# Kernel optimization log

Hardware: AMD Instinct MI355X
Metric: run time of the kernel (lower is better)

Reference implementation:

```python
import jax, jax.numpy as jnp
import numpy as np
import math

D_MODEL = 2048
NUM_HEADS = 32
NUM_KV_HEADS = 8
D_K = D_MODEL // NUM_HEADS  # 64
GROUPS = NUM_HEADS // NUM_KV_HEADS  # 4
WINDOW = 512
ROPE_BASE = 10000.0


def setup_inputs() -> dict:
    key = jax.random.key(0)
    ks = jax.random.split(key, 5)
    B, T = 2, 2048
    x = jax.random.normal(ks[0], (B, T, D_MODEL), dtype=jnp.float32)
    s = 0.02  # typical init scale to keep logits sane
    Wq = jax.random.normal(ks[1], (D_MODEL, D_MODEL), dtype=jnp.float32) * s
    Wk = jax.random.normal(ks[2], (NUM_KV_HEADS * D_K, D_MODEL), dtype=jnp.float32) * s
    Wv = jax.random.normal(ks[3], (NUM_KV_HEADS * D_K, D_MODEL), dtype=jnp.float32) * s
    Wo = jax.random.normal(ks[4], (D_MODEL, D_MODEL), dtype=jnp.float32) * s
    return {"x": x, "Wq": Wq, "Wk": Wk, "Wv": Wv, "Wo": Wo}


def _rotate_half(t):
    half = t.shape[-1] // 2
    return jnp.concatenate([-t[..., half:], t[..., :half]], axis=-1)


def _rope_cos_sin(T, dtype):
    inv_freq = 1.0 / (ROPE_BASE ** (jnp.arange(0, D_K, 2, dtype=jnp.float32) / D_K))
    pos = jnp.arange(T, dtype=jnp.float32)
    freqs = pos[:, None] * inv_freq[None, :]            # [T, D_K/2]
    emb = jnp.concatenate([freqs, freqs], axis=-1)       # [T, D_K]
    return jnp.cos(emb).astype(dtype)[None, None], jnp.sin(emb).astype(dtype)[None, None]


def reference(x, Wq, Wk, Wv, Wo):
    B, T, D = x.shape
    # Projections (nn.Linear: x @ W.T)
    Q = (x @ Wq.T).reshape(B, T, NUM_HEADS, D_K).transpose(0, 2, 1, 3)     # [B,H,T,dk]
    K = (x @ Wk.T).reshape(B, T, NUM_KV_HEADS, D_K).transpose(0, 2, 1, 3)  # [B,KV,T,dk]
    V = (x @ Wv.T).reshape(B, T, NUM_KV_HEADS, D_K).transpose(0, 2, 1, 3)
    # RoPE
    cos, sin = _rope_cos_sin(T, x.dtype)
    Q = Q * cos + _rotate_half(Q) * sin
    K = K * cos + _rotate_half(K) * sin
    # GQA: fold group dim into Q instead of repeat_interleave on K/V (same math)
    Qg = Q.reshape(B, NUM_KV_HEADS, GROUPS, T, D_K)
    scale = math.sqrt(D_K)
    scores = jnp.einsum('bhgqd,bhkd->bhgqk', Qg, K) / scale  # [B,KV,G,T,T]
    # sliding-window causal mask: valid iff 0 <= q_pos - k_pos < WINDOW
    pos = jnp.arange(T)
    dist = pos[:, None] - pos[None, :]
    win_mask = (dist < 0) | (dist >= WINDOW)
    scores = jnp.where(win_mask[None, None, None], -jnp.inf, scores)
    attn = jax.nn.softmax(scores, axis=-1)
    out = jnp.einsum('bhgqk,bhkd->bhgqd', attn, V)
    out = out.reshape(B, NUM_HEADS, T, D_K).transpose(0, 2, 1, 3).reshape(B, T, D)
    return out @ Wo.T
```

## Files before the change

kernel.cpp:

```cpp
#include <hip/hip_runtime.h>
#include <hip/hip_bf16.h>
#include <cstdint>
#include <cstddef>

typedef __attribute__((ext_vector_type(4))) float f32x4;
typedef __attribute__((ext_vector_type(8))) short bf16x8;
typedef __attribute__((ext_vector_type(4))) int i32x4;
typedef void __attribute__((address_space(1)))* as1_void_p;
typedef void __attribute__((address_space(3)))* as3_void_p;

#define T_SEQ 2048
#define D_MODEL 2048
#define NUM_HEADS 32
#define NUM_KV 8
#define GROUPS 4
#define DK 64
#define WINDOW 512
#define BATCH 2

#define NEG_BIG (-30000.0f)

__device__ __forceinline__ unsigned short f2b(float f) {
    unsigned int u = __builtin_bit_cast(unsigned int, f);
    u = (u + 0x7FFFu + ((u >> 16) & 1u)) >> 16;
    return (unsigned short)u;
}

__device__ __forceinline__ unsigned int cvtpk_bf16(float lo, float hi) {
    unsigned int r;
    asm("v_cvt_pk_bf16_f32 %0, %1, %2" : "=v"(r) : "v"(lo), "v"(hi));
    return r;
}

__device__ __forceinline__ void load_lds16(const void* g, void* l) {
    __builtin_amdgcn_global_load_lds((as1_void_p)(uintptr_t)g,
                                     (as3_void_p)(unsigned int)(uintptr_t)l,
                                     16, 0, 0);
}

#define CAST_N0 8388608
#define CAST_N1 12582912
#define CAST_N2 13631488
#define CAST_N3 14680064
#define CAST_N4 18874368
__global__ void cast_all_kernel(const float* __restrict__ x, const float* __restrict__ wq,
                                const float* __restrict__ wk, const float* __restrict__ wv,
                                const float* __restrict__ wo, unsigned short* __restrict__ dst) {
    int i = (blockIdx.x * blockDim.x + threadIdx.x) * 4;
    const int stride = gridDim.x * blockDim.x * 4;
    for (; i < CAST_N4; i += stride) {
        const float* src;
        int off;
        if (i < CAST_N0)      { src = x;  off = i; }
        else if (i < CAST_N1) { src = wq; off = i - CAST_N0; }
        else if (i < CAST_N2) { src = wk; off = i - CAST_N1; }
        else if (i < CAST_N3) { src = wv; off = i - CAST_N2; }
        else                  { src = wo; off = i - CAST_N3; }
        const float4 v = *(const float4*)(src + off);
        ushort4 o;
        o.x = f2b(v.x); o.y = f2b(v.y); o.z = f2b(v.z); o.w = f2b(v.w);
        *(ushort4*)(dst + i) = o;
    }
}

__global__ void rope_table_kernel(float* __restrict__ ct, float* __restrict__ st) {
    int i = blockIdx.x * blockDim.x + threadIdx.x;
    int t = i >> 5, j = i & 31;
    const float kln = 0.28782313662425556f;
    float inv = __expf(-(float)j * kln);
    if (j == 0) inv = 1.0f;
    float ang = (float)t * inv;
    float s, c;
    sincosf(ang, &s, &c);
    ct[i] = c; st[i] = s;
}


#define STAGE32(LDSOFF, SRC, ROWBASE, KCOL)                                    \
    { _Pragma("unroll") for (int u = 0; u < 2; ++u) {                          \
        const int gi = u * 512 + tid;                                          \
        const int row_ = gi >> 2, slot_ = gi & 3;                              \
        const int scol = (slot_ ^ ((row_ >> 1) & 3)) << 3;                     \
        load_lds16(SRC + (size_t)((ROWBASE) + row_) * 2048 + (KCOL) + scol,    \
                   (char*)&lds[LDSOFF] + gi * 16); } }

#define GEMM8_CORE(APTR, BPTR, TM, TN, AROWS, BROWS)                           \
    const int tid = threadIdx.x;                                               \
    const int lane = tid & 63;                                                 \
    const int wid = tid >> 6;                                                  \
    const int wr = wid >> 1, wc = wid & 1;                        \
    const int lrow = lane & 15;                                                \
    const int g = lane >> 4;                                                   \
    const int tile_m = (TM), tile_n = (TN);                                    \
    const int arow = tile_m * (AROWS), brow = tile_n * (BROWS);                \
    (void)brow;

__global__ __launch_bounds__(512, 2) void gemm_qkv_rope(
    const unsigned short* __restrict__ A, const unsigned short* __restrict__ Bw,
    const float* __restrict__ ct, const float* __restrict__ st,
    unsigned short* __restrict__ Qb, unsigned short* __restrict__ Kb,
    unsigned short* __restrict__ Vt) {
    __shared__ __align__(16) unsigned short lds[32768];
    const int bid = blockIdx.x;
    const int xcd = bid & 7;
    const int l = bid >> 3;
    const int stl = l >> 4;
    const int w = l & 15;
    const int tmD = xcd * 4 + (w >> 2);
    const int tnD = stl * 4 + (w & 3);

    GEMM8_CORE(A, Bw, tmD, tnD, 128, 128)

    const int srow = tid >> 2, sslot = tid & 3;
    const int scol0 = (sslot ^ ((srow >> 1) & 3)) << 3;

    f32x4 acc[2][4] = {};

#define QSTAGE(BUF, KCOL)                                                      \
    {                                                                          \
        load_lds16(A + (size_t)(arow + srow) * 2048 + (KCOL) + scol0,          \
                   (char*)&lds[(BUF) * 8192] + tid * 16);                      \
        load_lds16(Bw + (size_t)(tnD * 128 + srow) * 2048 + (KCOL) + scol0,    \
                   (char*)&lds[(BUF) * 8192 + 4096] + tid * 16);               \
    }

    QSTAGE(0, 0) QSTAGE(1, 32) QSTAGE(2, 64)
    asm volatile("s_waitcnt vmcnt(4)" ::: "memory");
    __builtin_amdgcn_sched_barrier(0);
    __builtin_amdgcn_s_barrier();

    for (int t = 0; t < 64; ++t) {
        const int cb = (t & 3) * 8192;
        const int sb = (t + 3) & 3;
        bf16x8 af[2], bfr[4];
#pragma unroll
        for (int m = 0; m < 2; ++m) {
            const int R = wr * 32 + m * 16 + lrow;
            af[m] = *(const bf16x8*)&lds[cb + R * 32 + ((g ^ ((R >> 1) & 3)) << 3)];
        }
#pragma unroll
        for (int n = 0; n < 4; ++n) {
            const int R = wc * 64 + n * 16 + lrow;
            bfr[n] = *(const bf16x8*)&lds[cb + 4096 + R * 32 + ((g ^ ((R >> 1) & 3)) << 3)];
        }
        if (t + 3 < 64) QSTAGE(sb, (t + 3) * 32)
        __builtin_amdgcn_s_barrier();
        asm volatile("s_waitcnt lgkmcnt(0)" ::: "memory");
        __builtin_amdgcn_sched_barrier(0);
        __builtin_amdgcn_s_setprio(1);
#pragma unroll
        for (int m = 0; m < 2; ++m)
#pragma unroll
            for (int n = 0; n < 4; ++n)
                acc[m][n] = __builtin_amdgcn_mfma_f32_16x16x32_bf16(af[m], bfr[n], acc[m][n], 0, 0, 0);
        __builtin_amdgcn_s_setprio(0);
        if (t < 63) { asm volatile("s_waitcnt vmcnt(4)" ::: "memory"); }
        else        { asm volatile("s_waitcnt vmcnt(0)" ::: "memory"); }
        __builtin_amdgcn_sched_barrier(0);
        __builtin_amdgcn_s_barrier();
    }
#undef QSTAGE

    const int hcol = tile_n * 2 + wc;
#pragma unroll
    for (int m = 0; m < 2; ++m) {
        const int row0 = tile_m * 128 + wr * 32 + m * 16 + g * 4;
        const int bb = row0 >> 11;
        const int t0 = row0 & 2047;
        if (hcol < 40) {
            const bool isQ = (hcol < 32);
            const float sc = isQ ? 0.125f : 1.0f;
            unsigned short* base = isQ
                ? (Qb + ((size_t)(bb * NUM_HEADS + hcol) * T_SEQ) * 64)
                : (Kb + ((size_t)(bb * NUM_KV + (hcol - 32)) * T_SEQ) * 64);
#pragma unroll
            for (int r = 0; r < 4; ++r) {
                const int t = t0 + r;
                unsigned short* dst = base + (size_t)t * 64;
#pragma unroll
                for (int n = 0; n < 2; ++n) {
                    const int j = n * 16 + lrow;
                    const float c = ct[t * 32 + j], s = st[t * 32 + j];
                    const float v0 = acc[m][n][r], v1 = acc[m][n + 2][r];
                    dst[j]      = f2b((v0 * c - v1 * s) * sc);
                    dst[j + 32] = f2b((v1 * c + v0 * s) * sc);
                }
            }
        } else {
            const int vh = hcol - 40;
            const int chunk = t0 >> 5, tk = t0 & 31;
            unsigned short* cbase = Vt + ((size_t)(bb * NUM_KV + vh) * 64 + chunk) * 2048 + tk;
#pragma unroll
            for (int n = 0; n < 4; ++n) {
                const int d = n * 16 + lrow;
                unsigned int u0 = cvtpk_bf16(acc[m][n][0], acc[m][n][1]);
                unsigned int u1 = cvtpk_bf16(acc[m][n][2], acc[m][n][3]);
                uint2 val; val.x = u0; val.y = u1;
                *(uint2*)(cbase + d * 32) = val;
            }
        }
    }
}

__global__ __launch_bounds__(512, 2) void gemm_bf16_nt(
    const unsigned short* __restrict__ A, const unsigned short* __restrict__ B,
    float* __restrict__ C) {
    __shared__ __align__(16) unsigned short lds[49152];
    const int bid = blockIdx.x;
    const int xcd = bid & 7;
    const int l = bid >> 3;
    const int stl = l >> 4;
    const int w = l & 15;
    const int tmD = xcd * 4 + (w >> 2);
    const int tnD = stl * 4 + (w & 3);

    const int tid = threadIdx.x;
    const int lane = tid & 63;
    const int wid = tid >> 6;
    const int wr = wid >> 2, wc = wid & 3;
    const int lrow = lane & 15;
    const int g = lane >> 4;
    const int tile_m = tmD, tile_n = tnD;
    const int arow = tile_m * 128, brow = tile_n * 256;

    const int srow = tid >> 2, sslot = tid & 3;
    const int scol = (sslot ^ ((srow >> 1) & 3)) << 3;

    f32x4 acc[4][4] = {};

#define OSTAGE(BUF, KCOL)                                                      \
    {                                                                          \
        load_lds16(A + (size_t)(arow + srow) * 2048 + (KCOL) + scol,           \
                   (char*)&lds[(BUF) * 12288] + tid * 16);                     \
        _Pragma("unroll") for (int u = 0; u < 2; ++u) {                        \
            const int gi = u * 512 + tid;                                      \
            const int br_ = gi >> 2, bs_ = gi & 3;                             \
            const int bc_ = (bs_ ^ ((br_ >> 1) & 3)) << 3;                     \
            load_lds16(B + (size_t)(brow + br_) * 2048 + (KCOL) + bc_,         \
                       (char*)&lds[(BUF) * 12288 + 4096] + gi * 16);           \
        }                                                                      \
    }

    OSTAGE(0, 0) OSTAGE(1, 32) OSTAGE(2, 64)
    asm volatile("s_waitcnt vmcnt(6)" ::: "memory");
    __builtin_amdgcn_sched_barrier(0);
    __builtin_amdgcn_s_barrier();

    for (int t = 0; t < 64; ++t) {
        const int cb = (t & 3) * 12288;
        const int sb = (t + 3) & 3;
        bf16x8 af[4], bfr[4];
#pragma unroll
        for (int m = 0; m < 4; ++m) {
            const int R = wr * 64 + m * 16 + lrow;
            af[m] = *(const bf16x8*)&lds[cb + R * 32 + ((g ^ ((R >> 1) & 3)) << 3)];
        }
#pragma unroll
        for (int n = 0; n < 4; ++n) {
            const int R = wc * 64 + n * 16 + lrow;
            bfr[n] = *(const bf16x8*)&lds[cb + 4096 + R * 32 + ((g ^ ((R >> 1) & 3)) << 3)];
        }
        if (t + 3 < 64) OSTAGE(sb, (t + 3) * 32)
        __builtin_amdgcn_s_barrier();
        asm volatile("s_waitcnt lgkmcnt(0)" ::: "memory");
        __builtin_amdgcn_sched_barrier(0);
        __builtin_amdgcn_s_setprio(1);
#pragma unroll
        for (int m = 0; m < 4; ++m)
#pragma unroll
            for (int n = 0; n < 4; ++n)
                acc[m][n] = __builtin_amdgcn_mfma_f32_16x16x32_bf16(af[m], bfr[n], acc[m][n], 0, 0, 0);
        __builtin_amdgcn_s_setprio(0);
        if (t < 63) { asm volatile("s_waitcnt vmcnt(6)" ::: "memory"); }
        else        { asm volatile("s_waitcnt vmcnt(0)" ::: "memory"); }
        __builtin_amdgcn_sched_barrier(0);
        __builtin_amdgcn_s_barrier();
    }
#undef OSTAGE

#pragma unroll
    for (int m = 0; m < 4; ++m)
#pragma unroll
        for (int n = 0; n < 4; ++n) {
            const int col = tile_n * 256 + wc * 64 + n * 16 + lrow;
#pragma unroll
            for (int r = 0; r < 4; ++r) {
                const int row = tile_m * 128 + wr * 64 + m * 16 + g * 4 + r;
                C[(size_t)row * 2048 + col] = acc[m][n][r];
            }
        }
}

__global__ __launch_bounds__(512, 2) void attn_kernel(
    const unsigned short* __restrict__ Qb, const unsigned short* __restrict__ Kb,
    const unsigned short* __restrict__ Vt, unsigned short* __restrict__ Oout) {
    __shared__ __align__(16) unsigned short lds[12288];
    const int tid = threadIdx.x;
    const int lane = tid & 63;
    const int wv = tid >> 6;
    const int g4 = wv & 3;
    const int tile = wv >> 2;
    const int bid = blockIdx.x;
    const int kvh = bid & 7;
    const int b = (bid >> 3) & 1;
    const int band = 63 - (bid >> 4);
    const int q0A = band * 32;
    const int q0w = q0A + tile * 16;
    const int h = kvh * 4 + g4;

    const int lq = lane & 15;
    const int g = lane >> 4;
    const int kq8 = g * 8;
    const int q = q0w + lq;

    const unsigned short* Qrow = Qb + ((size_t)((b * NUM_HEADS + h) * T_SEQ) + q) * 64;
    const bf16x8 qf0 = *(const bf16x8*)(Qrow + kq8);
    const bf16x8 qf1 = *(const bf16x8*)(Qrow + 32 + kq8);

    f32x4 acc[4] = {};
    float lrun = 0.0f;

    int kc_lo = q0A - (WINDOW - 1);
    if (kc_lo < 0) kc_lo = 0;
    kc_lo &= ~31;
    const int N = ((q0A - kc_lo) >> 5) + 1;

    const unsigned short* Kg = Kb + (size_t)(b * NUM_KV + kvh) * T_SEQ * 64
                                  + (size_t)kc_lo * 64;
    const unsigned short* Vg = Vt + (size_t)(b * NUM_KV + kvh) * 64 * T_SEQ
                                  + (size_t)(kc_lo >> 5) * 2048;

    const int perm = (lq >> 2) * 8 + (lq & 3);
#define SWZK(r) (((r & 3) | ((r >> 3) << 2)) & 7)
    const int koff0 = perm * 64 + ((g ^ SWZK(perm)) << 3);
    const int koff1 = perm * 64 + (((4 + g) ^ SWZK(perm)) << 3);
    const int perm4 = perm + 4;
    const int koff2 = perm4 * 64 + ((g ^ SWZK(perm4)) << 3);
    const int koff3 = perm4 * 64 + (((4 + g) ^ SWZK(perm4)) << 3);
    int voff[4];
#pragma unroll
    for (int nd = 0; nd < 4; ++nd)
        voff[nd] = 2048 + (nd * 16 + lq) * 32 + ((g ^ ((lq >> 1) & 3)) << 3);

#define STAGE(T, BUF)                                                          \
    {                                                                          \
        if (tid < 256) {                                                       \
            const int row_ = tid >> 3, ps = tid & 7;                           \
            const int ls = ps ^ SWZK(row_);                                    \
            load_lds16(Kg + (size_t)(T) * 2048 + row_ * 64 + ls * 8,           \
                       (char*)lds + (BUF) * 8192 + tid * 16);                  \
        } else {                                                               \
            const int gi = tid - 256;                                          \
            const int row_ = gi >> 2, ps = gi & 3;                             \
            const int ls = ps ^ ((row_ >> 1) & 3);                             \
            load_lds16(Vg + (size_t)(T) * 2048 + row_ * 32 + ls * 8,           \
                       (char*)lds + (BUF) * 8192 + 4096 + gi * 16);            \
        }                                                                      \
    }

    STAGE(0, 0)
    if (N > 1) {
        STAGE(1, 1)
        asm volatile("s_waitcnt vmcnt(1)" ::: "memory");
    } else {
        asm volatile("s_waitcnt vmcnt(0)" ::: "memory");
    }
    __builtin_amdgcn_sched_barrier(0);
    __builtin_amdgcn_s_barrier();

    int kb = 0;
    int sbuf = 2;
    for (int t = 0; t < N; ++t) {
        bf16x8 kf[4], vf[4];
        kf[0] = *(const bf16x8*)&lds[kb + koff0];
        kf[1] = *(const bf16x8*)&lds[kb + koff1];
        kf[2] = *(const bf16x8*)&lds[kb + koff2];
        kf[3] = *(const bf16x8*)&lds[kb + koff3];
#pragma unroll
        for (int nd = 0; nd < 4; ++nd) vf[nd] = *(const bf16x8*)&lds[kb + voff[nd]];
        if (t + 2 < N) STAGE(t + 2, sbuf)
        asm volatile("s_waitcnt lgkmcnt(0)" ::: "memory");
        __builtin_amdgcn_sched_barrier(0);

        const int kc = kc_lo + t * 32;
        f32x4 st2[2] = {};
        st2[0] = __builtin_amdgcn_mfma_f32_16x16x32_bf16(kf[0], qf0, st2[0], 0, 0, 0);
        st2[0] = __builtin_amdgcn_mfma_f32_16x16x32_bf16(kf[1], qf1, st2[0], 0, 0, 0);
        st2[1] = __builtin_amdgcn_mfma_f32_16x16x32_bf16(kf[2], qf0, st2[1], 0, 0, 0);
        st2[1] = __builtin_amdgcn_mfma_f32_16x16x32_bf16(kf[3], qf1, st2[1], 0, 0, 0);

        float s8[8];
#pragma unroll
        for (int tt = 0; tt < 2; ++tt)
#pragma unroll
            for (int r = 0; r < 4; ++r) s8[tt * 4 + r] = st2[tt][r];

        if (kc < q0w - 496 || kc > q0w - 31) {
#pragma unroll
            for (int i = 0; i < 8; ++i) {
                const int key = kc + g * 8 + ((i >> 2) << 2) + (i & 3);
                const int dist = q - key;
                if (dist < 0 || dist >= WINDOW) s8[i] = NEG_BIG;
            }
        }

        float p8[8];
        float ps = 0.0f;
#pragma unroll
        for (int i = 0; i < 8; ++i) {
            p8[i] = __expf(s8[i]);
            ps += p8[i];
        }
        lrun += ps;

        i32x4 pwi;
        pwi[0] = (int)cvtpk_bf16(p8[0], p8[1]);
        pwi[1] = (int)cvtpk_bf16(p8[2], p8[3]);
        pwi[2] = (int)cvtpk_bf16(p8[4], p8[5]);
        pwi[3] = (int)cvtpk_bf16(p8[6], p8[7]);
        const bf16x8 pw = __builtin_bit_cast(bf16x8, pwi);

#pragma unroll
        for (int nd = 0; nd < 4; ++nd)
            acc[nd] = __builtin_amdgcn_mfma_f32_16x16x32_bf16(vf[nd], pw, acc[nd], 0, 0, 0);

        if (t + 1 < N) {
            if (t + 2 < N) { asm volatile("s_waitcnt vmcnt(1)" ::: "memory"); }
            else           { asm volatile("s_waitcnt vmcnt(0)" ::: "memory"); }
            __builtin_amdgcn_sched_barrier(0);
            __builtin_amdgcn_s_barrier();
        }
        kb += 4096; if (kb == 12288) kb = 0;
        sbuf += 1;  if (sbuf == 3) sbuf = 0;
    }
#undef STAGE
#undef SWZK

    lrun += __shfl_xor(lrun, 16);
    lrun += __shfl_xor(lrun, 32);

    const float inv = 1.0f / lrun;
#pragma unroll
    for (int nd = 0; nd < 4; ++nd) {
        unsigned int u0 = cvtpk_bf16(acc[nd][0] * inv, acc[nd][1] * inv);
        unsigned int u1 = cvtpk_bf16(acc[nd][2] * inv, acc[nd][3] * inv);
        unsigned short* dst = Oout + ((size_t)(b * T_SEQ + q)) * D_MODEL + h * 64 + nd * 16 + g * 4;
        uint2 val; val.x = u0; val.y = u1;
        *(uint2*)dst = val;
    }
}

extern "C" void kernel_launch(void* const* d_in, const int* in_sizes, int n_in,
                              void* d_out, int out_size, void* d_ws, size_t ws_size,
                              hipStream_t stream) {
    const float* x = (const float*)d_in[0];
    const float* Wq = (const float*)d_in[1];
    const float* Wk = (const float*)d_in[2];
    const float* Wv = (const float*)d_in[3];
    const float* Wo = (const float*)d_in[4];
    float* out = (float*)d_out;

    char* ws = (char*)d_ws;
    size_t off = 0;
    auto alloc = [&](size_t bytes) -> char* {
        char* p = ws + off;
        off += (bytes + 255) & ~(size_t)255;
        return p;
    };
    unsigned short* xb   = (unsigned short*)alloc(8388608ull * 2);
    unsigned short* wcat = (unsigned short*)alloc(6291456ull * 2);
    unsigned short* wob  = (unsigned short*)alloc(4194304ull * 2);
    unsigned short* qb   = (unsigned short*)alloc(8388608ull * 2);
    unsigned short* kb   = (unsigned short*)alloc(2097152ull * 2);
    unsigned short* vt   = (unsigned short*)alloc(2097152ull * 2);
    unsigned short* attn = (unsigned short*)alloc(8388608ull * 2);
    float* ct            = (float*)alloc(65536ull * 4);
    float* st            = (float*)alloc(65536ull * 4);

    cast_all_kernel<<<2048, 256, 0, stream>>>(x, Wq, Wk, Wv, Wo, xb);
    rope_table_kernel<<<256, 256, 0, stream>>>(ct, st);

    gemm_qkv_rope<<<768, 512, 0, stream>>>(xb, wcat, ct, st, qb, kb, vt);

    attn_kernel<<<1024, 512, 0, stream>>>(qb, kb, vt, attn);

    gemm_bf16_nt<<<256, 512, 0, stream>>>(attn, wob, out);
}
```

Measured before the change: 153.6 us.

## Deepen attention K/V prefetch to four LDS buffers and raise occupancy bounds

The attention kernel's K/V staging ring grows from three to four LDS buffers, with tiles prefetched three steps ahead and the vmcnt waits adjusted to match. This is meant to hide more global load latency behind the MFMA and softmax work. Launch bounds for both the QKV GEMM and attention kernels are raised from 2 to 4 blocks per CU, which pushes the compiler to use fewer registers and may cause spills. The GEMM helper macros are also inlined, which does not change behaviour.

```diff
diff --git a/kernel.cpp b/kernel.cpp
--- a/kernel.cpp
+++ b/kernel.cpp
@@ -76,26 +76,7 @@
 }
 
 
-#define STAGE32(LDSOFF, SRC, ROWBASE, KCOL)                                    \
-    { _Pragma("unroll") for (int u = 0; u < 2; ++u) {                          \
-        const int gi = u * 512 + tid;                                          \
-        const int row_ = gi >> 2, slot_ = gi & 3;                              \
-        const int scol = (slot_ ^ ((row_ >> 1) & 3)) << 3;                     \
-        load_lds16(SRC + (size_t)((ROWBASE) + row_) * 2048 + (KCOL) + scol,    \
-                   (char*)&lds[LDSOFF] + gi * 16); } }
-
-#define GEMM8_CORE(APTR, BPTR, TM, TN, AROWS, BROWS)                           \
-    const int tid = threadIdx.x;                                               \
-    const int lane = tid & 63;                                                 \
-    const int wid = tid >> 6;                                                  \
-    const int wr = wid >> 1, wc = wid & 1;                        \
-    const int lrow = lane & 15;                                                \
-    const int g = lane >> 4;                                                   \
-    const int tile_m = (TM), tile_n = (TN);                                    \
-    const int arow = tile_m * (AROWS), brow = tile_n * (BROWS);                \
-    (void)brow;
-
-__global__ __launch_bounds__(512, 2) void gemm_qkv_rope(
+__global__ __launch_bounds__(512, 4) void gemm_qkv_rope(
     const unsigned short* __restrict__ A, const unsigned short* __restrict__ Bw,
     const float* __restrict__ ct, const float* __restrict__ st,
     unsigned short* __restrict__ Qb, unsigned short* __restrict__ Kb,
@@ -109,7 +90,14 @@
     const int tmD = xcd * 4 + (w >> 2);
     const int tnD = stl * 4 + (w & 3);
 
-    GEMM8_CORE(A, Bw, tmD, tnD, 128, 128)
+    const int tid = threadIdx.x;
+    const int lane = tid & 63;
+    const int wid = tid >> 6;
+    const int wr = wid >> 1, wc = wid & 1;
+    const int lrow = lane & 15;
+    const int g = lane >> 4;
+    const int tile_m = tmD, tile_n = tnD;
+    const int arow = tile_m * 128;
 
     const int srow = tid >> 2, sslot = tid & 3;
     const int scol0 = (sslot ^ ((srow >> 1) & 3)) << 3;
@@ -291,10 +279,10 @@
         }
 }
 
-__global__ __launch_bounds__(512, 2) void attn_kernel(
+__global__ __launch_bounds__(512, 4) void attn_kernel(
     const unsigned short* __restrict__ Qb, const unsigned short* __restrict__ Kb,
     const unsigned short* __restrict__ Vt, unsigned short* __restrict__ Oout) {
-    __shared__ __align__(16) unsigned short lds[12288];
+    __shared__ __align__(16) unsigned short lds[16384];
     const int tid = threadIdx.x;
     const int lane = tid & 63;
     const int wv = tid >> 6;
@@ -359,18 +347,16 @@
     }
 
     STAGE(0, 0)
-    if (N > 1) {
-        STAGE(1, 1)
-        asm volatile("s_waitcnt vmcnt(1)" ::: "memory");
-    } else {
-        asm volatile("s_waitcnt vmcnt(0)" ::: "memory");
-    }
+    if (N > 1) STAGE(1, 1)
+    if (N > 2) STAGE(2, 2)
+    if (N > 2)      { asm volatile("s_waitcnt vmcnt(2)" ::: "memory"); }
+    else if (N > 1) { asm volatile("s_waitcnt vmcnt(1)" ::: "memory"); }
+    else            { asm volatile("s_waitcnt vmcnt(0)" ::: "memory"); }
     __builtin_amdgcn_sched_barrier(0);
     __builtin_amdgcn_s_barrier();
 
-    int kb = 0;
-    int sbuf = 2;
     for (int t = 0; t < N; ++t) {
+        const int kb = (t & 3) * 4096;
         bf16x8 kf[4], vf[4];
         kf[0] = *(const bf16x8*)&lds[kb + koff0];
         kf[1] = *(const bf16x8*)&lds[kb + koff1];
@@ -378,7 +364,7 @@
         kf[3] = *(const bf16x8*)&lds[kb + koff3];
 #pragma unroll
         for (int nd = 0; nd < 4; ++nd) vf[nd] = *(const bf16x8*)&lds[kb + voff[nd]];
-        if (t + 2 < N) STAGE(t + 2, sbuf)
+        if (t + 3 < N) STAGE(t + 3, (t + 3) & 3)
         asm volatile("s_waitcnt lgkmcnt(0)" ::: "memory");
         __builtin_amdgcn_sched_barrier(0);
 
@@ -425,13 +411,12 @@
             acc[nd] = __builtin_amdgcn_mfma_f32_16x16x32_bf16(vf[nd], pw, acc[nd], 0, 0, 0);
 
         if (t + 1 < N) {
-            if (t + 2 < N) { asm volatile("s_waitcnt vmcnt(1)" ::: "memory"); }
-            else           { asm volatile("s_waitcnt vmcnt(0)" ::: "memory"); }
+            if (t + 3 < N)      { asm volatile("s_waitcnt vmcnt(2)" ::: "memory"); }
+            else if (t + 2 < N) { asm volatile("s_waitcnt vmcnt(1)" ::: "memory"); }
+            else                { asm volatile("s_waitcnt vmcnt(0)" ::: "memory"); }
             __builtin_amdgcn_sched_barrier(0);
             __builtin_amdgcn_s_barrier();
         }
-        kb += 4096; if (kb == 12288) kb = 0;
-        sbuf += 1;  if (sbuf == 3) sbuf = 0;
     }
 #undef STAGE
 #undef SWZK
```

Result: no change. 154.5 us (+0.6%).
